# Kernel tuning notes

Hardware: AMD Instinct MI355X
Metric: run time of the kernel (lower is better)

The kernel has to match this reference:

```python
import jax, jax.numpy as jnp
import numpy as np

B, T_IN, C_IN = 64, 1000, 4
F, K, POOL = 320, 26, 13
H = 320          # GRU units per direction
T_CONV = T_IN - K + 1   # 975
T_POOL = T_CONV // POOL  # 75
FLAT = T_POOL * 2 * H    # 48000
D1, D2 = 2000, 301


def setup_inputs() -> dict:
    key = jax.random.key(0)
    ks = jax.random.split(key, 12)
    s = 0.05
    return {
        "inputs": jax.random.normal(ks[0], (B, T_IN, C_IN), jnp.float32),
        "conv_w": jax.random.normal(ks[1], (K, C_IN, F), jnp.float32) * s,
        "conv_b": jnp.zeros((F,), jnp.float32),
        "gru_fw_k": jax.random.normal(ks[2], (F, 3 * H), jnp.float32) * s,
        "gru_fw_rk": jax.random.normal(ks[3], (H, 3 * H), jnp.float32) * s,
        "gru_fw_b": jnp.zeros((2, 3 * H), jnp.float32),
        "gru_bw_k": jax.random.normal(ks[4], (F, 3 * H), jnp.float32) * s,
        "gru_bw_rk": jax.random.normal(ks[5], (H, 3 * H), jnp.float32) * s,
        "gru_bw_b": jnp.zeros((2, 3 * H), jnp.float32),
        "w1": jax.random.normal(ks[6], (FLAT, D1), jnp.float32) * 0.01,
        "b1": jnp.zeros((D1,), jnp.float32),
        "w2": jax.random.normal(ks[7], (D1, D2), jnp.float32) * s,
        "b2": jnp.zeros((D2,), jnp.float32),
    }


def _gru_scan(xs, k, rk, b):
    # xs: (T, B, C) -> ys: (T, B, H). Keras GRU, reset_after=True, inference.
    bi, br = b[0], b[1]
    h0 = jnp.zeros((xs.shape[1], rk.shape[0]), xs.dtype)

    def step(h, x):
        mx = x @ k + bi                      # (B, 3H)
        mi = h @ rk + br                     # (B, 3H)
        xz, xr, xh = jnp.split(mx, 3, axis=-1)
        hz, hr, hh = jnp.split(mi, 3, axis=-1)
        z = jax.nn.sigmoid(xz + hz)
        r = jax.nn.sigmoid(xr + hr)
        cand = jnp.tanh(xh + r * hh)
        hn = z * h + (1.0 - z) * cand
        return hn, hn

    _, ys = jax.lax.scan(step, h0, xs)
    return ys


def _forward(inputs, conv_w, conv_b, gru_fw_k, gru_fw_rk, gru_fw_b,
             gru_bw_k, gru_bw_rk, gru_bw_b, w1, b1, w2, b2):
    # Conv1D valid + relu: (B, 975, 320)
    x = jax.lax.conv_general_dilated(
        inputs, conv_w, window_strides=(1,), padding="VALID",
        dimension_numbers=("NWC", "WIO", "NWC"))
    x = jax.nn.relu(x + conv_b)
    # MaxPool1D pool=13 stride=13 valid: (B, 75, 320)
    x = jax.lax.reduce_window(
        x, -jnp.inf, jax.lax.max, (1, POOL, 1), (1, POOL, 1), "VALID")
    # Bidirectional GRU, return_sequences, concat merge
    xs = jnp.transpose(x, (1, 0, 2))  # (T, B, C)
    fw = _gru_scan(xs, gru_fw_k, gru_fw_rk, gru_fw_b)            # (T, B, H)
    bw = _gru_scan(xs[::-1], gru_bw_k, gru_bw_rk, gru_bw_b)[::-1]
    y = jnp.concatenate([fw, bw], axis=-1)                        # (T, B, 2H)
    y = jnp.transpose(y, (1, 0, 2)).reshape(inputs.shape[0], -1)  # (B, 48000)
    y = jax.nn.relu(y @ w1 + b1)
    return jax.nn.sigmoid(y @ w2 + b2)


def reference(inputs, conv_w, conv_b, gru_fw_k, gru_fw_rk, gru_fw_b,
              gru_bw_k, gru_bw_rk, gru_bw_b, w1, b1, w2, b2):
    return _forward(inputs, conv_w, conv_b, gru_fw_k, gru_fw_rk, gru_fw_b,
                    gru_bw_k, gru_bw_rk, gru_bw_b, w1, b1, w2, b2)
```

## Files before the change

kernel.cpp:

```cpp
#include <hip/hip_runtime.h>

typedef _Float16 f16;
typedef _Float16 f16x4 __attribute__((ext_vector_type(4)));
typedef _Float16 f16x8 __attribute__((ext_vector_type(8)));
typedef float f32x4 __attribute__((ext_vector_type(4)));

#define B_ 64
#define TIN 1000
#define CIN 4
#define F_ 320
#define KW 26
#define TCONV 975
#define TPOOL 75
#define H_ 320
#define G3 960
#define FLAT 48000
#define D1 2000
#define D2 301


__global__ void k_prep_in(const float* __restrict__ inp, f16* __restrict__ o) {
    int i = blockIdx.x * 256 + threadIdx.x;
    if (i < B_ * TIN * CIN) o[i] = (f16)inp[i];
}

__global__ void k_prep_w(const float* __restrict__ w, f16* __restrict__ o) {
    int i = blockIdx.x * 256 + threadIdx.x;
    if (i >= 20 * 4 * 64 * 8) return;
    int e = i & 7, l = (i >> 3) & 63, t1 = i >> 9;
    int kf = t1 & 3, nt = t1 >> 2;
    int k = kf * 32 + 8 * (l >> 4) + e;
    int kk = k >> 2, c = k & 3, f = nt * 16 + (l & 15);
    o[i] = (f16)((kk < KW) ? w[(kk * CIN + c) * F_ + f] : 0.f);
}

__global__ void k_prep_k(const float* __restrict__ fw, const float* __restrict__ bw,
                         f16* __restrict__ o) {
    int i = blockIdx.x * 256 + threadIdx.x;
    if (i >= 2 * 60 * 10 * 64 * 8) return;
    int e = i & 7, l = (i >> 3) & 63, t1 = i >> 9;
    int kf = t1 % 10; int t2 = t1 / 10;
    int nt = t2 % 60; int d = t2 / 60;
    int k = kf * 32 + 8 * (l >> 4) + e;
    int n = nt * 16 + (l & 15);
    const float* src = d ? bw : fw;
    o[i] = (f16)src[k * G3 + n];
}

__global__ __launch_bounds__(256) void k_conv(const f16* __restrict__ in16,
                                              const f16* __restrict__ wswz,
                                              const float* __restrict__ convb,
                                              f16* __restrict__ xpool) {
    int pg = blockIdx.x, b = blockIdx.y, ntb = blockIdx.z;
    int tid = threadIdx.x, w = tid >> 6, l = tid & 63;
    int g = l >> 4, lm = l & 15;
    __shared__ float convbuf[64 * 72];

    int r = 16 * w + lm;
    int t = pg * 52 + r;
    int tt = t > (TCONV - 1) ? (TCONV - 1) : t;

    f32x4 acc[4] = {};
#pragma unroll
    for (int kf = 0; kf < 4; ++kf) {
        int kk0 = kf * 8 + 2 * g;
        int flat = b * 4000 + (tt + kk0) * 4;
        if (flat > B_ * TIN * CIN - 8) flat = B_ * TIN * CIN - 8;
        f16x4 lo = *(const f16x4*)(in16 + flat);
        f16x4 hi = *(const f16x4*)(in16 + flat + 4);
        f16x8 a;
        a[0] = lo[0]; a[1] = lo[1]; a[2] = lo[2]; a[3] = lo[3];
        a[4] = hi[0]; a[5] = hi[1]; a[6] = hi[2]; a[7] = hi[3];
#pragma unroll
        for (int nt = 0; nt < 4; ++nt) {
            int ntg = ntb * 4 + nt;
            f16x8 bf = *(const f16x8*)(wswz + (size_t)((ntg * 4 + kf) * 64 + l) * 8);
            acc[nt] = __builtin_amdgcn_mfma_f32_16x16x32_f16(a, bf, acc[nt], 0, 0, 0);
        }
    }
#pragma unroll
    for (int nt = 0; nt < 4; ++nt) {
        int f = (ntb * 4 + nt) * 16 + lm;
        float cb = convb[f];
#pragma unroll
        for (int j = 0; j < 4; ++j) {
            int row = 16 * w + 4 * g + j;
            float v = acc[nt][j] + cb;
            convbuf[row * 72 + nt * 16 + lm] = v > 0.f ? v : 0.f;
        }
    }
    __syncthreads();
    int pl = tid >> 6, n = tid & 63;
    int p = pg * 4 + pl;
    if (p < TPOOL) {
        float m = 0.f;
#pragma unroll
        for (int q = 0; q < 13; ++q) m = fmaxf(m, convbuf[(pl * 13 + q) * 72 + n]);
        xpool[((size_t)p * B_ + b) * F_ + ntb * 64 + n] = (f16)m;
    }
}

__global__ __launch_bounds__(256) void k_mx(const f16* __restrict__ xpool,
                                            const f16* __restrict__ kswz,
                                            const float* __restrict__ fwb,
                                            const float* __restrict__ bwb,
                                            float* __restrict__ mx) {
    int t = blockIdx.x, ntb = blockIdx.y, d = blockIdx.z;
    int tid = threadIdx.x, w = tid >> 6, l = tid & 63;
    int g = l >> 4, lm = l & 15;
    int b = 16 * w + lm;

    f16x8 a[10];
    const f16* ap = xpool + ((size_t)t * B_ + b) * F_;
#pragma unroll
    for (int kf = 0; kf < 10; ++kf) a[kf] = *(const f16x8*)(ap + kf * 32 + 8 * g);

    const f16* kp = kswz + (size_t)d * 60 * 10 * 64 * 8;
    const float* gb = d ? bwb : fwb;

    f32x4 acc[4] = {};
#pragma unroll
    for (int kf = 0; kf < 10; ++kf) {
        f16x8 af = a[kf];
#pragma unroll
        for (int nt = 0; nt < 4; ++nt) {
            int ntg = ntb * 4 + nt;
            f16x8 bf = *(const f16x8*)(kp + (size_t)((ntg * 10 + kf) * 64 + l) * 8);
            acc[nt] = __builtin_amdgcn_mfma_f32_16x16x32_f16(af, bf, acc[nt], 0, 0, 0);
        }
    }
    float* op = mx + ((size_t)d * TPOOL + t) * B_ * G3;
#pragma unroll
    for (int nt = 0; nt < 4; ++nt) {
        int n = (ntb * 4 + nt) * 16 + lm;
        float bias = gb[n] + (n < 640 ? gb[G3 + n] : 0.f);
#pragma unroll
        for (int j = 0; j < 4; ++j) {
            int bb = 16 * w + 4 * g + j;
            op[(size_t)bb * G3 + n] = acc[nt][j] + bias;
        }
    }
}

__global__ __launch_bounds__(1024) void k_gru(const f16* __restrict__ rkswz,
                                              const float* __restrict__ mx,
                                              const float* __restrict__ fwb,
                                              const float* __restrict__ bwb,
                                              f16* __restrict__ a16) {
    int d = blockIdx.x >> 2, g4 = blockIdx.x & 3;
    int tid = threadIdx.x;
    int w = tid >> 6, l = tid & 63, g = l >> 4, lm = l & 15;
    __shared__ f16 h16[16 * 328];
    __shared__ float h32[16 * 320];
    __shared__ float mi[16 * 964];
    for (int i = tid; i < 16 * 328; i += 1024) h16[i] = (f16)0.f;
    for (int i = tid; i < 16 * 320; i += 1024) h32[i] = 0.f;

    int ub = tid >> 6;
    int ul = tid & 63;
    const float* gb = d ? bwb : fwb;
    float brh[5];
#pragma unroll
    for (int j = 0; j < 5; ++j) brh[j] = gb[G3 + 640 + ul + 64 * j];

    const f16* rkp = rkswz + (size_t)d * 60 * 10 * 64 * 8;
    bool mfma_wave = (w < 12);
    __syncthreads();

    for (int s = 0; s < TPOOL; ++s) {
        int t = d ? (TPOOL - 1 - s) : s;
        const float* mrow = mx + (((size_t)d * TPOOL + t) * B_ + (g4 * 16 + ub)) * G3;
        float pz[5], pr[5], ph[5];
#pragma unroll
        for (int j = 0; j < 5; ++j) {
            int u = ul + 64 * j;
            pz[j] = mrow[u]; pr[j] = mrow[320 + u]; ph[j] = mrow[640 + u];
        }
        if (mfma_wave) {
            f16x8 a[10];
#pragma unroll
            for (int kf = 0; kf < 10; ++kf)
                a[kf] = *(const f16x8*)(&h16[lm * 328 + kf * 32 + 8 * g]);
            f32x4 acc[5] = {};
#pragma unroll
            for (int kf = 0; kf < 10; ++kf) {
                f16x8 af = a[kf];
#pragma unroll
                for (int i = 0; i < 5; ++i) {
                    int nt = w * 5 + i;
                    f16x8 bf = *(const f16x8*)(rkp + (size_t)((nt * 10 + kf) * 64 + l) * 8);
                    acc[i] = __builtin_amdgcn_mfma_f32_16x16x32_f16(af, bf, acc[i], 0, 0, 0);
                }
            }
#pragma unroll
            for (int i = 0; i < 5; ++i) {
                int nt = w * 5 + i;
#pragma unroll
                for (int j = 0; j < 4; ++j)
                    mi[(4 * g + j) * 964 + nt * 16 + lm] = acc[i][j];
            }
        }
        __syncthreads();
#pragma unroll
        for (int j = 0; j < 5; ++j) {
            int u = ul + 64 * j;
            float miz = mi[ub * 964 + u];
            float mir = mi[ub * 964 + 320 + u];
            float mih = mi[ub * 964 + 640 + u];
            float z = 1.f / (1.f + __expf(-(pz[j] + miz)));
            float rr = 1.f / (1.f + __expf(-(pr[j] + mir)));
            float hhat = ph[j] + rr * (mih + brh[j]);
            float e2 = __expf(2.f * hhat);
            float cand = 1.f - 2.f / (e2 + 1.f);
            float ho = h32[ub * 320 + u];
            float hn = z * ho + (1.f - z) * cand;
            h32[ub * 320 + u] = hn;
            h16[ub * 328 + u] = (f16)hn;
            a16[(size_t)(g4 * 16 + ub) * FLAT + t * 640 + d * 320 + u] = (f16)hn;
        }
        __syncthreads();
    }
}

__global__ __launch_bounds__(256) void k_fc1(const f16* __restrict__ a16,
                                             const float* __restrict__ w1,
                                             float* __restrict__ part) {
    int kc = blockIdx.x, ntb = blockIdx.y;
    int tid = threadIdx.x, w = tid >> 6, l = tid & 63;
    int g = l >> 4, lm = l & 15;
    __shared__ f16 bstage[64 * 40];
    int n0 = ntb * 64;
    int kbase = kc * 1920;
    f32x4 acc[4] = {};
    const f16* ap = a16 + (size_t)(16 * w + lm) * FLAT + kbase + 8 * g;

    for (int ks = 0; ks < 60; ++ks) {
        int k0 = kbase + ks * 32;
#pragma unroll
        for (int ii = 0; ii < 2; ++ii) {
            int lin = ii * 256 + tid;
            int kk = lin >> 4;
            int nn = (lin & 15) * 4;
            int ng = n0 + nn;
            const float* wp = w1 + (size_t)(k0 + kk) * D1 + ng;
            float vx, vy, vz, vw;
            if (ng + 3 < D1) { float4 v = *(const float4*)wp; vx = v.x; vy = v.y; vz = v.z; vw = v.w; }
            else {
                vx = ng     < D1 ? wp[0] : 0.f;
                vy = ng + 1 < D1 ? wp[1] : 0.f;
                vz = ng + 2 < D1 ? wp[2] : 0.f;
                vw = ng + 3 < D1 ? wp[3] : 0.f;
            }
            bstage[(nn    ) * 40 + kk] = (f16)vx;
            bstage[(nn + 1) * 40 + kk] = (f16)vy;
            bstage[(nn + 2) * 40 + kk] = (f16)vz;
            bstage[(nn + 3) * 40 + kk] = (f16)vw;
        }
        __syncthreads();
        f16x8 a = *(const f16x8*)(ap + ks * 32);
#pragma unroll
        for (int nt = 0; nt < 4; ++nt) {
            f16x8 bf = *(const f16x8*)(&bstage[(nt * 16 + lm) * 40 + 8 * g]);
            acc[nt] = __builtin_amdgcn_mfma_f32_16x16x32_f16(a, bf, acc[nt], 0, 0, 0);
        }
        __syncthreads();
    }
#pragma unroll
    for (int nt = 0; nt < 4; ++nt) {
        int n = n0 + nt * 16 + lm;
        if (n < D1) {
#pragma unroll
            for (int j = 0; j < 4; ++j) {
                int bb = 16 * w + 4 * g + j;
                part[((size_t)kc * B_ + bb) * D1 + n] = acc[nt][j];
            }
        }
    }
}

__global__ __launch_bounds__(384) void k_fc2(const float* __restrict__ part,
                                             const float* __restrict__ b1,
                                             const float* __restrict__ w2,
                                             const float* __restrict__ b2,
                                             float* __restrict__ out) {
    int b = blockIdx.x;
    int tid = threadIdx.x;
    __shared__ float y1f[D1];
    for (int n = tid; n < D1; n += 384) {
        float s = b1[n];
#pragma unroll
        for (int kc = 0; kc < 25; ++kc) s += part[((size_t)kc * B_ + b) * D1 + n];
        y1f[n] = s > 0.f ? s : 0.f;
    }
    __syncthreads();
    if (tid < D2) {
        float acc = b2[tid];
#pragma unroll 4
        for (int n = 0; n < D1; ++n) acc += y1f[n] * w2[n * D2 + tid];
        out[b * D2 + tid] = 1.f / (1.f + __expf(-acc));
    }
}

extern "C" void kernel_launch(void* const* d_in, const int* in_sizes, int n_in,
                              void* d_out, int out_size, void* d_ws, size_t ws_size,
                              hipStream_t stream) {
    const float* inp   = (const float*)d_in[0];
    const float* convw = (const float*)d_in[1];
    const float* convb = (const float*)d_in[2];
    const float* fwk   = (const float*)d_in[3];
    const float* fwrk  = (const float*)d_in[4];
    const float* fwb   = (const float*)d_in[5];
    const float* bwk   = (const float*)d_in[6];
    const float* bwrk  = (const float*)d_in[7];
    const float* bwb   = (const float*)d_in[8];
    const float* w1    = (const float*)d_in[9];
    const float* b1    = (const float*)d_in[10];
    const float* w2    = (const float*)d_in[11];
    const float* b2    = (const float*)d_in[12];
    float* out = (float*)d_out;

    char* ws = (char*)d_ws;
    size_t off = 0;
    auto alloc = [&](size_t bytes) { size_t o = off; off += (bytes + 255) & ~(size_t)255; return o; };
    f16*   in16  = (f16*)(ws + alloc((size_t)B_ * TIN * CIN * 2));
    f16*   wswz  = (f16*)(ws + alloc((size_t)20 * 4 * 64 * 8 * 2));
    f16*   kswz  = (f16*)(ws + alloc((size_t)2 * 60 * 10 * 64 * 8 * 2));
    f16*   rkswz = (f16*)(ws + alloc((size_t)2 * 60 * 10 * 64 * 8 * 2));
    f16*   xpool = (f16*)(ws + alloc((size_t)TPOOL * B_ * F_ * 2));
    float* mx    = (float*)(ws + alloc((size_t)2 * TPOOL * B_ * G3 * 4));
    f16*   a16   = (f16*)(ws + alloc((size_t)B_ * FLAT * 2));
    float* part  = (float*)(ws + alloc((size_t)25 * B_ * D1 * 4));
    (void)ws_size; (void)in_sizes; (void)n_in; (void)out_size;

    k_prep_in<<<dim3((B_ * TIN * CIN + 255) / 256), 256, 0, stream>>>(inp, in16);
    k_prep_w<<<dim3((20 * 4 * 64 * 8 + 255) / 256), 256, 0, stream>>>(convw, wswz);
    k_prep_k<<<dim3((2 * 60 * 10 * 64 * 8 + 255) / 256), 256, 0, stream>>>(fwk, bwk, kswz);
    k_prep_k<<<dim3((2 * 60 * 10 * 64 * 8 + 255) / 256), 256, 0, stream>>>(fwrk, bwrk, rkswz);
    k_conv<<<dim3(19, 64, 5), 256, 0, stream>>>(in16, wswz, convb, xpool);
    k_mx<<<dim3(75, 15, 2), 256, 0, stream>>>(xpool, kswz, fwb, bwb, mx);
    k_gru<<<dim3(8), 1024, 0, stream>>>(rkswz, mx, fwb, bwb, a16);
    k_fc1<<<dim3(25, 32), 256, 0, stream>>>(a16, w1, part);
    k_fc2<<<dim3(64), 384, 0, stream>>>(part, b1, w2, b2, out);
}
```

Baseline: 1.627 ms.

## Split GRU recurrence across blocks with global-memory hidden-state exchange and counters

The GRU recurrence is spread over 40 blocks instead of 8, five blocks per (direction, batch-group), each owning 64 hidden units. Each block keeps its recurrent-weight slice in registers and reads the full previous hidden state from a global staging buffer. Blocks synchronise every timestep through acquire/release atomic counters. This removes the per-step recurrent-weight reloads from global/L2 and spreads the MFMA work across more CUs. In exchange it adds inter-block spin-waits and global-memory round trips on every step, and it relies on all 40 blocks being resident at once.

New measurement: 2.624 ms. 1.61x slower.

```diff
diff --git a/kernel.cpp b/kernel.cpp
--- a/kernel.cpp
+++ b/kernel.cpp
@@ -17,11 +17,17 @@
 #define FLAT 48000
 #define D1 2000
 #define D2 301
+#define NSPLIT 5
 
 
 __global__ void k_prep_in(const float* __restrict__ inp, f16* __restrict__ o) {
     int i = blockIdx.x * 256 + threadIdx.x;
     if (i < B_ * TIN * CIN) o[i] = (f16)inp[i];
+}
+
+__global__ void k_zero_cnt(int* __restrict__ cnt) {
+    int i = blockIdx.x * 256 + threadIdx.x;
+    if (i < 2 * 4 * 80) cnt[i] = 0;
 }
 
 __global__ void k_prep_w(const float* __restrict__ w, f16* __restrict__ o) {
@@ -142,83 +148,92 @@
     }
 }
 
-__global__ __launch_bounds__(1024) void k_gru(const f16* __restrict__ rkswz,
-                                              const float* __restrict__ mx,
-                                              const float* __restrict__ fwb,
-                                              const float* __restrict__ bwb,
-                                              f16* __restrict__ a16) {
-    int d = blockIdx.x >> 2, g4 = blockIdx.x & 3;
+__global__ __launch_bounds__(1024) void k_gru2(const f16* __restrict__ rkswz,
+                                               const float* __restrict__ mx,
+                                               const float* __restrict__ fwb,
+                                               const float* __restrict__ bwb,
+                                               f16* __restrict__ hst,
+                                               int* __restrict__ cnt,
+                                               f16* __restrict__ a16) {
+    int nb = blockIdx.x;
+    int bg = blockIdx.y;
+    int d  = blockIdx.z;
     int tid = threadIdx.x;
     int w = tid >> 6, l = tid & 63, g = l >> 4, lm = l & 15;
-    __shared__ f16 h16[16 * 328];
-    __shared__ float h32[16 * 320];
-    __shared__ float mi[16 * 964];
-    for (int i = tid; i < 16 * 328; i += 1024) h16[i] = (f16)0.f;
-    for (int i = tid; i < 16 * 320; i += 1024) h32[i] = 0.f;
+    int grp = d * 4 + bg;
+
+    __shared__ float mi[16 * 196];
+
+    f16x8 bfr[10];
+    const f16* rkp = rkswz + (size_t)d * 60 * 10 * 64 * 8;
+    if (w < 12) {
+        int ntg = (w >> 2) * 20 + nb * 4 + (w & 3);
+#pragma unroll
+        for (int kf = 0; kf < 10; ++kf)
+            bfr[kf] = *(const f16x8*)(rkp + (size_t)((ntg * 10 + kf) * 64 + l) * 8);
+    }
 
     int ub = tid >> 6;
-    int ul = tid & 63;
+    int uu = tid & 63;
+    int ug = nb * 64 + uu;
     const float* gb = d ? bwb : fwb;
-    float brh[5];
-#pragma unroll
-    for (int j = 0; j < 5; ++j) brh[j] = gb[G3 + 640 + ul + 64 * j];
-
-    const f16* rkp = rkswz + (size_t)d * 60 * 10 * 64 * 8;
-    bool mfma_wave = (w < 12);
-    __syncthreads();
+    float brh = gb[G3 + 640 + ug];
+    float hprev = 0.f;
+
+    const f16* hsg = hst + (size_t)grp * 76 * 16 * 320;
+    int* cg = cnt + grp * 80;
 
     for (int s = 0; s < TPOOL; ++s) {
         int t = d ? (TPOOL - 1 - s) : s;
-        const float* mrow = mx + (((size_t)d * TPOOL + t) * B_ + (g4 * 16 + ub)) * G3;
-        float pz[5], pr[5], ph[5];
-#pragma unroll
-        for (int j = 0; j < 5; ++j) {
-            int u = ul + 64 * j;
-            pz[j] = mrow[u]; pr[j] = mrow[320 + u]; ph[j] = mrow[640 + u];
-        }
-        if (mfma_wave) {
-            f16x8 a[10];
-#pragma unroll
-            for (int kf = 0; kf < 10; ++kf)
-                a[kf] = *(const f16x8*)(&h16[lm * 328 + kf * 32 + 8 * g]);
-            f32x4 acc[5] = {};
-#pragma unroll
-            for (int kf = 0; kf < 10; ++kf) {
-                f16x8 af = a[kf];
-#pragma unroll
-                for (int i = 0; i < 5; ++i) {
-                    int nt = w * 5 + i;
-                    f16x8 bf = *(const f16x8*)(rkp + (size_t)((nt * 10 + kf) * 64 + l) * 8);
-                    acc[i] = __builtin_amdgcn_mfma_f32_16x16x32_f16(af, bf, acc[i], 0, 0, 0);
-                }
+        const float* mrow = mx + (((size_t)d * TPOOL + t) * B_ + (bg * 16 + ub)) * G3;
+        float pz = mrow[ug], pr = mrow[320 + ug], ph = mrow[640 + ug];
+
+        if (s > 0) {
+            if (tid == 0) {
+                while (__hip_atomic_load(&cg[s], __ATOMIC_ACQUIRE,
+                                         __HIP_MEMORY_SCOPE_AGENT) < NSPLIT) {}
             }
-#pragma unroll
-            for (int i = 0; i < 5; ++i) {
-                int nt = w * 5 + i;
+            __syncthreads();
+            __threadfence();
+            if (w < 12) {
+                const f16* ha = hsg + ((size_t)s * 16 + lm) * 320;
+                f16x8 a[10];
+#pragma unroll
+                for (int kf = 0; kf < 10; ++kf)
+                    a[kf] = *(const f16x8*)(ha + kf * 32 + 8 * g);
+                f32x4 acc = {};
+#pragma unroll
+                for (int kf = 0; kf < 10; ++kf)
+                    acc = __builtin_amdgcn_mfma_f32_16x16x32_f16(a[kf], bfr[kf], acc, 0, 0, 0);
 #pragma unroll
                 for (int j = 0; j < 4; ++j)
-                    mi[(4 * g + j) * 964 + nt * 16 + lm] = acc[i][j];
+                    mi[(4 * g + j) * 196 + w * 16 + lm] = acc[j];
             }
         }
         __syncthreads();
-#pragma unroll
-        for (int j = 0; j < 5; ++j) {
-            int u = ul + 64 * j;
-            float miz = mi[ub * 964 + u];
-            float mir = mi[ub * 964 + 320 + u];
-            float mih = mi[ub * 964 + 640 + u];
-            float z = 1.f / (1.f + __expf(-(pz[j] + miz)));
-            float rr = 1.f / (1.f + __expf(-(pr[j] + mir)));
-            float hhat = ph[j] + rr * (mih + brh[j]);
-            float e2 = __expf(2.f * hhat);
-            float cand = 1.f - 2.f / (e2 + 1.f);
-            float ho = h32[ub * 320 + u];
-            float hn = z * ho + (1.f - z) * cand;
-            h32[ub * 320 + u] = hn;
-            h16[ub * 328 + u] = (f16)hn;
-            a16[(size_t)(g4 * 16 + ub) * FLAT + t * 640 + d * 320 + u] = (f16)hn;
-        }
+
+        float miz = 0.f, mir = 0.f, mih = 0.f;
+        if (s > 0) {
+            miz = mi[ub * 196 + uu];
+            mir = mi[ub * 196 + 64 + uu];
+            mih = mi[ub * 196 + 128 + uu];
+        }
+        float z = 1.f / (1.f + __expf(-(pz + miz)));
+        float rr = 1.f / (1.f + __expf(-(pr + mir)));
+        float hhat = ph + rr * (mih + brh);
+        float e2 = __expf(2.f * hhat);
+        float cand = 1.f - 2.f / (e2 + 1.f);
+        float hn = z * hprev + (1.f - z) * cand;
+        hprev = hn;
+
+        ((f16*)hsg)[((size_t)(s + 1) * 16 + ub) * 320 + ug] = (f16)hn;
+        a16[(size_t)(bg * 16 + ub) * FLAT + t * 640 + d * 320 + ug] = (f16)hn;
+
+        __threadfence();
         __syncthreads();
+        if (tid == 0)
+            __hip_atomic_fetch_add(&cg[s + 1], 1, __ATOMIC_RELEASE,
+                                   __HIP_MEMORY_SCOPE_AGENT);
     }
 }
 
@@ -330,15 +345,18 @@
     float* mx    = (float*)(ws + alloc((size_t)2 * TPOOL * B_ * G3 * 4));
     f16*   a16   = (f16*)(ws + alloc((size_t)B_ * FLAT * 2));
     float* part  = (float*)(ws + alloc((size_t)25 * B_ * D1 * 4));
+    f16*   hst   = (f16*)(ws + alloc((size_t)8 * 76 * 16 * 320 * 2));
+    int*   cnt   = (int*)(ws + alloc((size_t)2 * 4 * 80 * 4));
     (void)ws_size; (void)in_sizes; (void)n_in; (void)out_size;
 
     k_prep_in<<<dim3((B_ * TIN * CIN + 255) / 256), 256, 0, stream>>>(inp, in16);
+    k_zero_cnt<<<dim3(3), 256, 0, stream>>>(cnt);
     k_prep_w<<<dim3((20 * 4 * 64 * 8 + 255) / 256), 256, 0, stream>>>(convw, wswz);
     k_prep_k<<<dim3((2 * 60 * 10 * 64 * 8 + 255) / 256), 256, 0, stream>>>(fwk, bwk, kswz);
     k_prep_k<<<dim3((2 * 60 * 10 * 64 * 8 + 255) / 256), 256, 0, stream>>>(fwrk, bwrk, rkswz);
     k_conv<<<dim3(19, 64, 5), 256, 0, stream>>>(in16, wswz, convb, xpool);
     k_mx<<<dim3(75, 15, 2), 256, 0, stream>>>(xpool, kswz, fwb, bwb, mx);
-    k_gru<<<dim3(8), 1024, 0, stream>>>(rkswz, mx, fwb, bwb, a16);
+    k_gru2<<<dim3(NSPLIT, 4, 2), 1024, 0, stream>>>(rkswz, mx, fwb, bwb, hst, cnt, a16);
     k_fc1<<<dim3(25, 32), 256, 0, stream>>>(a16, w1, part);
     k_fc2<<<dim3(64), 384, 0, stream>>>(part, b1, w2, b2, out);
 }
```
